# Kernel optimization log

Hardware: AMD Instinct MI355X
Metric: run time of the kernel (lower is better)

## Reference

```python
import jax, jax.numpy as jnp
import numpy as np


def setup_inputs() -> dict:
    key = jax.random.key(0)
    kx, kq, kk, kv = jax.random.split(key, 4)
    d_model, d_head = 1024, 64
    x = jax.random.normal(kx, (4, 4096, d_model), dtype=jnp.float32)
    scale = 1.0 / np.sqrt(d_model)
    Wq = jax.random.normal(kq, (d_model, d_head), dtype=jnp.float32) * scale
    Wk = jax.random.normal(kk, (d_model, d_head), dtype=jnp.float32) * scale
    Wv = jax.random.normal(kv, (d_model, d_head), dtype=jnp.float32) * scale
    return {"x": x, "Wq": Wq, "Wk": Wk, "Wv": Wv}


def reference(x, Wq, Wk, Wv):
    # x: [B, S, D]; Wq/Wk/Wv: [D, H]
    d_head = Wq.shape[-1]
    Q = jnp.einsum('bsd,dh->bsh', x, Wq)
    K = jnp.einsum('bsd,dh->bsh', x, Wk)
    V = jnp.einsum('bsd,dh->bsh', x, Wv)
    scores = jnp.einsum('bqh,bkh->bqk', Q, K) / jnp.sqrt(jnp.float32(d_head))
    S = x.shape[1]
    causal = jnp.tril(jnp.ones((S, S), dtype=bool))  # [S, S]
    scores = jnp.where(causal, scores, -jnp.inf)
    weights = jax.nn.softmax(scores, axis=-1)  # [B, S, S]
    return jnp.einsum('bqk,bkh->bqh', weights, V)
```

## Files before the change

kernel.cpp:

```cpp
#include <hip/hip_runtime.h>

#define D_MODEL 1024
#define D_HEAD  64
#define SEQ     4096
#define BATCH   4
#define M_TOT   (BATCH * SEQ)
#define LOG2E   1.44269504088896f
#define MFIX_L2 17.3123404906676f
#define CHUNK   4

typedef __bf16 bf16;
typedef bf16  bf16x8 __attribute__((ext_vector_type(8)));
typedef float f32x4  __attribute__((ext_vector_type(4)));

#define MFMA(a, b, c) __builtin_amdgcn_mfma_f32_16x16x32_bf16(a, b, c, 0, 0, 0)

#define QKV_OFF  0
#define OBUF_OFF 6291456
#define LBUF_OFF 10485760
#define WT_OFF   10551296
#define VT_OFF   10944512

__global__ void prep_kernel(const float* __restrict__ Wq, const float* __restrict__ Wk,
                            const float* __restrict__ Wv, bf16* __restrict__ Wt,
                            float4* __restrict__ zp, int n4)
{
    const int bx = blockIdx.x;
    const int t  = threadIdx.x;
    if (bx < 48) {
        __shared__ bf16 tr[64][72];
        const int wm = bx >> 4, kt = bx & 15, k0 = kt * 64;
        const float* W = (wm == 0) ? Wq : (wm == 1) ? Wk : Wv;
        const int kr = t >> 2, nb = (t & 3) * 16;
        #pragma unroll
        for (int j = 0; j < 4; j++) {
            float4 wrow = *(const float4*)(W + (size_t)(k0 + kr) * D_HEAD + nb + j * 4);
            tr[nb + j * 4 + 0][kr] = (bf16)wrow.x;
            tr[nb + j * 4 + 1][kr] = (bf16)wrow.y;
            tr[nb + j * 4 + 2][kr] = (bf16)wrow.z;
            tr[nb + j * 4 + 3][kr] = (bf16)wrow.w;
        }
        __syncthreads();
        const int n = t >> 2, kc = (t & 3) * 8;
        bf16* dst = Wt + (size_t)(wm * 64 + n) * D_MODEL + k0;
        #pragma unroll
        for (int h = 0; h < 2; h++) {
            bf16x8 v;
            #pragma unroll
            for (int j = 0; j < 8; j++) v[j] = tr[n][kc + h * 32 + j];
            *(bf16x8*)(dst + kc + h * 32) = v;
        }
    } else {
        int i = (bx - 48) * 256 + t;
        if (i < n4) zp[i] = float4{0.f, 0.f, 0.f, 0.f};
    }
}

#define XP 40

__global__ __launch_bounds__(512) void proj_kernel(
    const float* __restrict__ x, const bf16* __restrict__ Wt,
    bf16* __restrict__ qkv)
{
    __shared__ __align__(16) bf16 xs[2][2][64][XP];
    __shared__ __align__(16) bf16 ws[2][2][192][XP];
    __shared__ float red[64][193];

    const int t    = threadIdx.x;
    const int w    = t >> 6;
    const int g    = w >> 2;
    const int nw   = w & 3;
    const int lane = t & 63;
    const int quad = lane >> 4;
    const int l15  = lane & 15;
    const int row0 = blockIdx.x * 64;
    const int kb   = g * 512;

    const int tg   = t & 255;
    const int xrow = tg >> 2, xkq = (tg & 3) * 8;

    const float* xg = x + (size_t)(row0 + xrow) * D_MODEL + kb + xkq;

    f32x4 acc[12] = {};

    float4 xa, xb;
    bf16x8 wtv[3];

    auto load_regs = [&](int c) {
        xa = *(const float4*)(xg + c * 32);
        xb = *(const float4*)(xg + c * 32 + 4);
        #pragma unroll
        for (int it = 0; it < 3; it++) {
            int id = tg + it * 256, n = id >> 2, kk8 = (id & 3) * 8;
            wtv[it] = *(const bf16x8*)(Wt + (size_t)n * D_MODEL + kb + c * 32 + kk8);
        }
    };
    auto store_lds = [&](int p) {
        bf16x8 xv;
        xv[0] = (bf16)xa.x; xv[1] = (bf16)xa.y; xv[2] = (bf16)xa.z; xv[3] = (bf16)xa.w;
        xv[4] = (bf16)xb.x; xv[5] = (bf16)xb.y; xv[6] = (bf16)xb.z; xv[7] = (bf16)xb.w;
        *(bf16x8*)&xs[p][g][xrow][xkq] = xv;
        #pragma unroll
        for (int it = 0; it < 3; it++) {
            int id = tg + it * 256, n = id >> 2, kk8 = (id & 3) * 8;
            *(bf16x8*)&ws[p][g][n][kk8] = wtv[it];
        }
    };

    load_regs(0);
    store_lds(0);
    load_regs(1);
    __syncthreads();

    int p = 0;
    for (int c = 0; c < 16; c++) {
        bf16x8 af[4], bfr[3];
        #pragma unroll
        for (int rg = 0; rg < 4; rg++)
            af[rg] = *(bf16x8*)&xs[p][g][rg * 16 + l15][quad * 8];
        #pragma unroll
        for (int j = 0; j < 3; j++)
            bfr[j] = *(bf16x8*)&ws[p][g][nw * 48 + j * 16 + l15][quad * 8];
        #pragma unroll
        for (int rg = 0; rg < 4; rg++)
            #pragma unroll
            for (int j = 0; j < 3; j++)
                acc[rg * 3 + j] = MFMA(af[rg], bfr[j], acc[rg * 3 + j]);

        if (c + 1 < 16) {
            store_lds(p ^ 1);
            if (c + 2 < 16) load_regs(c + 2);
        }
        __syncthreads();
        p ^= 1;
    }

    if (g == 1) {
        #pragma unroll
        for (int rg = 0; rg < 4; rg++)
            #pragma unroll
            for (int j = 0; j < 3; j++)
                #pragma unroll
                for (int r = 0; r < 4; r++)
                    red[rg * 16 + quad * 4 + r][nw * 48 + j * 16 + l15] =
                        acc[rg * 3 + j][r];
    }
    __syncthreads();
    if (g == 0) {
        #pragma unroll
        for (int rg = 0; rg < 4; rg++)
            #pragma unroll
            for (int j = 0; j < 3; j++) {
                const int col = nw * 48 + j * 16 + l15;
                const int wm = col >> 6, h = col & 63;
                const float sc = (wm == 0) ? 0.125f : 1.0f;
                bf16* outp = qkv + (size_t)wm * M_TOT * D_HEAD;
                #pragma unroll
                for (int r = 0; r < 4; r++) {
                    const int row = rg * 16 + quad * 4 + r;
                    float s = acc[rg * 3 + j][r] + red[row][col];
                    outp[(size_t)(row0 + row) * D_HEAD + h] = (bf16)(s * sc);
                }
            }
    }
}

__global__ void vtrans_kernel(const bf16* __restrict__ qkv, bf16* __restrict__ vt)
{
    __shared__ bf16 trs[64][72];
    const bf16* Vsec = qkv + (size_t)2 * M_TOT * D_HEAD;
    const int t  = threadIdx.x;
    const int m0 = blockIdx.x * 64;
    const int b  = m0 >> 12, s0 = m0 & (SEQ - 1);

    #pragma unroll
    for (int half = 0; half < 2; half++) {
        const int ml = (t >> 3) + half * 32, hc = t & 7;
        bf16x8 v = *(const bf16x8*)(Vsec + (size_t)(m0 + ml) * D_HEAD + hc * 8);
        #pragma unroll
        for (int j = 0; j < 8; j++) trs[hc * 8 + j][ml] = v[j];
    }
    __syncthreads();
    #pragma unroll
    for (int half = 0; half < 2; half++) {
        const int hl = (t >> 3) + half * 32, sc = t & 7;
        bf16x8 v;
        #pragma unroll
        for (int j = 0; j < 8; j++) v[j] = trs[hl][sc * 8 + j];
        *(bf16x8*)(vt + ((size_t)b * D_HEAD + hl) * SEQ + s0 + sc * 8) = v;
    }
}

#define TS 72

__global__ __launch_bounds__(256) void attn_kernel(
    const bf16* __restrict__ qkv, const bf16* __restrict__ vt,
    float* __restrict__ o_buf, float* __restrict__ l_buf)
{
    const int i = blockIdx.x;
    const int c = blockIdx.y;
    const int b = blockIdx.z;
    const int ntiles = i + 1;
    const int tile0  = c * CHUNK;
    if (tile0 >= ntiles) return;
    const int tile1 = min(tile0 + CHUNK, ntiles);

    __shared__ __align__(16) bf16 Ks[64][TS];
    __shared__ __align__(16) bf16 Vs[64][TS];
    __shared__ __align__(16) bf16 Ps[4][16][TS];

    const bf16* Q = qkv;
    const bf16* K = qkv + (size_t)M_TOT * D_HEAD;

    const int t    = threadIdx.x;
    const int wv   = t >> 6;
    const int lane = t & 63;
    const int quad = lane >> 4;
    const int l15  = lane & 15;
    const int qb   = i * 64;
    const size_t base  = (size_t)b * SEQ * D_HEAD;
    const bf16* vtb = vt + (size_t)b * D_HEAD * SEQ;

    bf16x8 qf0, qf1;
    {
        const bf16* qr = Q + base + (size_t)(qb + wv * 16 + l15) * D_HEAD;
        qf0 = *(const bf16x8*)(qr + quad * 8);
        qf1 = *(const bf16x8*)(qr + 32 + quad * 8);
    }

    f32x4 o[4] = {};
    float l_r[4] = {};
    const int qw0 = qb + wv * 16;

    const int dr  = t >> 2;
    const int kq8 = (t & 3) * 8;

    bf16x8 kr0, kr1, vr0, vr1;
    {
        const bf16* kp = K + base + (size_t)(tile0 * 64 + dr) * D_HEAD;
        kr0 = *(const bf16x8*)(kp + kq8);
        kr1 = *(const bf16x8*)(kp + kq8 + 32);
        const bf16* vp = vtb + (size_t)dr * SEQ + tile0 * 64;
        vr0 = *(const bf16x8*)(vp + kq8);
        vr1 = *(const bf16x8*)(vp + kq8 + 32);
    }

    for (int tile = tile0; tile < tile1; tile++) {
        const int kk0 = tile * 64;
        *(bf16x8*)&Ks[dr][kq8]      = kr0;
        *(bf16x8*)&Ks[dr][kq8 + 32] = kr1;
        *(bf16x8*)&Vs[dr][kq8]      = vr0;
        *(bf16x8*)&Vs[dr][kq8 + 32] = vr1;
        __syncthreads();

        if (tile + 1 < tile1) {
            const bf16* kp = K + base + (size_t)((tile + 1) * 64 + dr) * D_HEAD;
            kr0 = *(const bf16x8*)(kp + kq8);
            kr1 = *(const bf16x8*)(kp + kq8 + 32);
            const bf16* vp = vtb + (size_t)dr * SEQ + (tile + 1) * 64;
            vr0 = *(const bf16x8*)(vp + kq8);
            vr1 = *(const bf16x8*)(vp + kq8 + 32);
        }

        f32x4 sc4[4];
        #pragma unroll
        for (int kt = 0; kt < 4; kt++) {
            f32x4 z = {};
            z = MFMA(qf0, *(bf16x8*)&Ks[kt * 16 + l15][quad * 8],      z);
            z = MFMA(qf1, *(bf16x8*)&Ks[kt * 16 + l15][32 + quad * 8], z);
            sc4[kt] = z;
        }

        const bool need_mask = (tile == i);

        #pragma unroll
        for (int r = 0; r < 4; r++) {
            #pragma unroll
            for (int kt = 0; kt < 4; kt++) {
                float s = sc4[kt][r];
                if (need_mask && (kk0 + kt * 16 + l15 > qw0 + quad * 4 + r))
                    s = -1e30f;
                float p = __builtin_amdgcn_exp2f(fmaf(s, LOG2E, -MFIX_L2));
                l_r[r] += p;
                Ps[wv][quad * 4 + r][kt * 16 + l15] = (bf16)p;
            }
        }
        __syncthreads();

        #pragma unroll
        for (int c2 = 0; c2 < 2; c2++) {
            bf16x8 pa = *(bf16x8*)&Ps[wv][l15][c2 * 32 + quad * 8];
            #pragma unroll
            for (int t4 = 0; t4 < 4; t4++) {
                bf16x8 vb = *(bf16x8*)&Vs[t4 * 16 + l15][c2 * 32 + quad * 8];
                o[t4] = MFMA(pa, vb, o[t4]);
            }
        }
        __syncthreads();
    }

    const int mrow0 = b * SEQ + qw0;
    #pragma unroll
    for (int r = 0; r < 4; r++) {
        float ls = l_r[r];
        #pragma unroll
        for (int sh = 1; sh < 16; sh <<= 1)
            ls += __shfl_xor(ls, sh, 64);
        if (l15 == 0)
            atomicAdd(&l_buf[mrow0 + quad * 4 + r], ls);
        const size_t orow = (size_t)(mrow0 + quad * 4 + r) * D_HEAD;
        #pragma unroll
        for (int t4 = 0; t4 < 4; t4++)
            atomicAdd(&o_buf[orow + t4 * 16 + l15], o[t4][r]);
    }
}

__global__ void norm_kernel(const float4* __restrict__ o_buf,
                            const float* __restrict__ l_buf,
                            float4* __restrict__ out)
{
    int gid = blockIdx.x * 256 + threadIdx.x;
    int m = gid >> 4;
    float inv = 1.0f / l_buf[m];
    float4 v = o_buf[gid];
    out[gid] = float4{v.x * inv, v.y * inv, v.z * inv, v.w * inv};
}

extern "C" void kernel_launch(void* const* d_in, const int* in_sizes, int n_in,
                              void* d_out, int out_size, void* d_ws, size_t ws_size,
                              hipStream_t stream) {
    const float* x  = (const float*)d_in[0];
    const float* Wq = (const float*)d_in[1];
    const float* Wk = (const float*)d_in[2];
    const float* Wv = (const float*)d_in[3];

    bf16*  qkv   = (bf16*)((char*)d_ws + QKV_OFF);
    float* o_buf = (float*)((char*)d_ws + OBUF_OFF);
    float* l_buf = (float*)((char*)d_ws + LBUF_OFF);
    bf16*  Wt    = (bf16*)((char*)d_ws + WT_OFF);
    bf16*  vt    = (bf16*)((char*)d_ws + VT_OFF);

    const int zero4 = (M_TOT * 65) / 4;
    const int zblocks = (zero4 + 255) / 256;
    prep_kernel<<<48 + zblocks, 256, 0, stream>>>(Wq, Wk, Wv, Wt,
                                                  (float4*)o_buf, zero4);
    proj_kernel<<<M_TOT / 64, 512, 0, stream>>>(x, Wt, qkv);
    vtrans_kernel<<<M_TOT / 64, 256, 0, stream>>>(qkv, vt);
    attn_kernel<<<dim3(SEQ / 64, SEQ / 64 / CHUNK, BATCH), 256, 0, stream>>>(
        qkv, vt, o_buf, l_buf);
    norm_kernel<<<M_TOT * 16 / 256, 256, 0, stream>>>((const float4*)o_buf, l_buf,
                                                      (float4*)d_out);
}
```

Measured before the change: 160.1 us.

## Double-buffer K/V tiles in LDS, drop per-tile barriers, double chunk size

Stores K/V into two alternating LDS buffers so the next tile is written after the PV matmul, and prefetches two tiles ahead, leaving one block barrier per tile instead of three. The barrier between writing P and reading it is replaced with an LDS waitcnt, relying on each wave reading only its own P rows. It also splits the masked diagonal tile from unmasked tiles and doubles CHUNK, which halves atomic output traffic and block count but lowers parallelism. LDS use grows, which may reduce occupancy.

```diff
diff --git a/kernel.cpp b/kernel.cpp
--- a/kernel.cpp
+++ b/kernel.cpp
@@ -7,7 +7,7 @@
 #define M_TOT   (BATCH * SEQ)
 #define LOG2E   1.44269504088896f
 #define MFIX_L2 17.3123404906676f
-#define CHUNK   4
+#define CHUNK   8
 
 typedef __bf16 bf16;
 typedef bf16  bf16x8 __attribute__((ext_vector_type(8)));
@@ -205,8 +205,8 @@
     if (tile0 >= ntiles) return;
     const int tile1 = min(tile0 + CHUNK, ntiles);
 
-    __shared__ __align__(16) bf16 Ks[64][TS];
-    __shared__ __align__(16) bf16 Vs[64][TS];
+    __shared__ __align__(16) bf16 Ks[2][64][TS];
+    __shared__ __align__(16) bf16 Vs[2][64][TS];
     __shared__ __align__(16) bf16 Ps[4][16][TS];
 
     const bf16* Q = qkv;
@@ -236,67 +236,82 @@
     const int kq8 = (t & 3) * 8;
 
     bf16x8 kr0, kr1, vr0, vr1;
-    {
-        const bf16* kp = K + base + (size_t)(tile0 * 64 + dr) * D_HEAD;
+    auto load_kv = [&](int tile) {
+        const bf16* kp = K + base + (size_t)(tile * 64 + dr) * D_HEAD;
         kr0 = *(const bf16x8*)(kp + kq8);
         kr1 = *(const bf16x8*)(kp + kq8 + 32);
-        const bf16* vp = vtb + (size_t)dr * SEQ + tile0 * 64;
+        const bf16* vp = vtb + (size_t)dr * SEQ + tile * 64;
         vr0 = *(const bf16x8*)(vp + kq8);
         vr1 = *(const bf16x8*)(vp + kq8 + 32);
-    }
-
+    };
+    auto store_kv = [&](int p) {
+        *(bf16x8*)&Ks[p][dr][kq8]      = kr0;
+        *(bf16x8*)&Ks[p][dr][kq8 + 32] = kr1;
+        *(bf16x8*)&Vs[p][dr][kq8]      = vr0;
+        *(bf16x8*)&Vs[p][dr][kq8 + 32] = vr1;
+    };
+
+    load_kv(tile0);
+    store_kv(0);
+    if (tile0 + 1 < tile1) load_kv(tile0 + 1);
+    __syncthreads();
+
+    int p = 0;
     for (int tile = tile0; tile < tile1; tile++) {
         const int kk0 = tile * 64;
-        *(bf16x8*)&Ks[dr][kq8]      = kr0;
-        *(bf16x8*)&Ks[dr][kq8 + 32] = kr1;
-        *(bf16x8*)&Vs[dr][kq8]      = vr0;
-        *(bf16x8*)&Vs[dr][kq8 + 32] = vr1;
-        __syncthreads();
-
-        if (tile + 1 < tile1) {
-            const bf16* kp = K + base + (size_t)((tile + 1) * 64 + dr) * D_HEAD;
-            kr0 = *(const bf16x8*)(kp + kq8);
-            kr1 = *(const bf16x8*)(kp + kq8 + 32);
-            const bf16* vp = vtb + (size_t)dr * SEQ + (tile + 1) * 64;
-            vr0 = *(const bf16x8*)(vp + kq8);
-            vr1 = *(const bf16x8*)(vp + kq8 + 32);
-        }
 
         f32x4 sc4[4];
         #pragma unroll
         for (int kt = 0; kt < 4; kt++) {
             f32x4 z = {};
-            z = MFMA(qf0, *(bf16x8*)&Ks[kt * 16 + l15][quad * 8],      z);
-            z = MFMA(qf1, *(bf16x8*)&Ks[kt * 16 + l15][32 + quad * 8], z);
+            z = MFMA(qf0, *(bf16x8*)&Ks[p][kt * 16 + l15][quad * 8],      z);
+            z = MFMA(qf1, *(bf16x8*)&Ks[p][kt * 16 + l15][32 + quad * 8], z);
             sc4[kt] = z;
         }
 
-        const bool need_mask = (tile == i);
-
-        #pragma unroll
-        for (int r = 0; r < 4; r++) {
-            #pragma unroll
-            for (int kt = 0; kt < 4; kt++) {
-                float s = sc4[kt][r];
-                if (need_mask && (kk0 + kt * 16 + l15 > qw0 + quad * 4 + r))
-                    s = -1e30f;
-                float p = __builtin_amdgcn_exp2f(fmaf(s, LOG2E, -MFIX_L2));
-                l_r[r] += p;
-                Ps[wv][quad * 4 + r][kt * 16 + l15] = (bf16)p;
+        if (tile == i) {
+            #pragma unroll
+            for (int r = 0; r < 4; r++) {
+                #pragma unroll
+                for (int kt = 0; kt < 4; kt++) {
+                    float s = sc4[kt][r];
+                    if (kk0 + kt * 16 + l15 > qw0 + quad * 4 + r)
+                        s = -1e30f;
+                    float pe = __builtin_amdgcn_exp2f(fmaf(s, LOG2E, -MFIX_L2));
+                    l_r[r] += pe;
+                    Ps[wv][quad * 4 + r][kt * 16 + l15] = (bf16)pe;
+                }
             }
-        }
-        __syncthreads();
+        } else {
+            #pragma unroll
+            for (int r = 0; r < 4; r++) {
+                #pragma unroll
+                for (int kt = 0; kt < 4; kt++) {
+                    float pe = __builtin_amdgcn_exp2f(
+                        fmaf(sc4[kt][r], LOG2E, -MFIX_L2));
+                    l_r[r] += pe;
+                    Ps[wv][quad * 4 + r][kt * 16 + l15] = (bf16)pe;
+                }
+            }
+        }
+        asm volatile("s_waitcnt lgkmcnt(0)" ::: "memory");
 
         #pragma unroll
         for (int c2 = 0; c2 < 2; c2++) {
             bf16x8 pa = *(bf16x8*)&Ps[wv][l15][c2 * 32 + quad * 8];
             #pragma unroll
             for (int t4 = 0; t4 < 4; t4++) {
-                bf16x8 vb = *(bf16x8*)&Vs[t4 * 16 + l15][c2 * 32 + quad * 8];
+                bf16x8 vb = *(bf16x8*)&Vs[p][t4 * 16 + l15][c2 * 32 + quad * 8];
                 o[t4] = MFMA(pa, vb, o[t4]);
             }
         }
-        __syncthreads();
+
+        if (tile + 1 < tile1) {
+            store_kv(p ^ 1);
+            if (tile + 2 < tile1) load_kv(tile + 2);
+            __syncthreads();
+        }
+        p ^= 1;
     }
 
     const int mrow0 = b * SEQ + qw0;
```

Measured after the change: 150.8 us. -5.8%, faster.
